# Performance work log

Measured on AMD Instinct MI355X. Metric: run time of the kernel, lower is better.

Reference implementation:

```python
import jax, jax.numpy as jnp
import numpy as np

N_NODES = 50000
N_EDGES = 800000
D_IN = 64
H1 = 64
H2 = 64
N_CLASSES = 10
N_GRAPHS = 500


def setup_inputs() -> dict:
    key = jax.random.key(0)
    ks = jax.random.split(key, 9)
    x = jax.random.normal(ks[0], (N_NODES, D_IN), dtype=jnp.float32)
    edge_index = jax.random.randint(ks[1], (2, N_EDGES), 0, N_NODES, dtype=jnp.int64)
    batch = jnp.sort(jax.random.randint(ks[2], (N_NODES,), 0, N_GRAPHS, dtype=jnp.int64))
    # Linear params (Kaiming-uniform-ish scale)
    def lin(k, fin, fout):
        kw, kb = jax.random.split(k)
        s = 1.0 / np.sqrt(fin)
        W = jax.random.uniform(kw, (fin, fout), minval=-s, maxval=s, dtype=jnp.float32)
        b = jax.random.uniform(kb, (fout,), minval=-s, maxval=s, dtype=jnp.float32)
        return W, b
    W1, b1 = lin(ks[3], D_IN, H1)
    W2, b2 = lin(ks[4], H1, H2)
    W3, b3 = lin(ks[5], H2, N_CLASSES)
    return {"x": x, "edge_index": edge_index, "batch": batch,
            "W1": W1, "b1": b1, "W2": W2, "b2": b2, "W3": W3, "b3": b3}


def _gin_conv(h, src, dst, W, b, eps=0.0):
    # sum aggregation of neighbor messages: msg[i] = sum_{(j->i)} h[j]
    agg = jax.ops.segment_sum(h[src], dst, num_segments=N_NODES)
    return ((1.0 + eps) * h + agg) @ W + b


def reference(x, edge_index, batch, W1, b1, W2, b2, W3, b3):
    src, dst = edge_index[0], edge_index[1]
    h = jax.nn.relu(_gin_conv(x, src, dst, W1, b1))
    h = jax.nn.relu(_gin_conv(h, src, dst, W2, b2))
    # global mean pool over graphs
    sums = jax.ops.segment_sum(h, batch, num_segments=N_GRAPHS)
    cnt = jax.ops.segment_sum(jnp.ones((N_NODES,), dtype=h.dtype), batch, num_segments=N_GRAPHS)
    pooled = sums / jnp.maximum(cnt, 1.0)[:, None]
    return pooled @ W3 + b3
```

## Files before the change

### kernel.cpp

```cpp
#include <hip/hip_runtime.h>
#include <hip/hip_bf16.h>
#include <hip/hip_fp16.h>


#define N_FEAT 64
#define CHUNK 4096
#define CAP 6144

typedef _Float16 f16;
typedef _Float16 half8 __attribute__((ext_vector_type(8)));
typedef float float4v __attribute__((ext_vector_type(4)));
typedef unsigned short u16;

__device__ inline f16 cvt_f16(float v) { return (f16)v; }
__device__ inline f16 cvt_f16(f16 v) { return v; }

template <typename TIN>
__device__ __forceinline__ void gemm_body(const TIN* __restrict__ X, const float* __restrict__ W,
                                          f16* __restrict__ Z, int nrows, int bidx, char* smemc) {
    f16 (*sX)[72] = (f16 (*)[72])smemc;
    f16 (*sWT)[72] = (f16 (*)[72])(smemc + 64 * 72 * sizeof(f16));
    int t = threadIdx.x;
    int base = bidx * 64;
    for (int idx = t; idx < 4096; idx += 256) {
        int k = idx >> 6, n = idx & 63;
        sWT[n][k] = (f16)W[idx];
    }
    for (int idx = t; idx < 4096; idx += 256) {
        int r = idx >> 6, c = idx & 63;
        int row = base + r;
        sX[r][c] = (row < nrows) ? cvt_f16(X[(size_t)row * 64 + c]) : (f16)0.f;
    }
    __syncthreads();
    int wave = t >> 6;
    int lane = t & 63;
    int quad = lane >> 4;
    int m16 = lane & 15;
    half8 a0 = *(const half8*)&sX[wave * 16 + m16][quad * 8];
    half8 a1 = *(const half8*)&sX[wave * 16 + m16][32 + quad * 8];
    float4v acc[4];
#pragma unroll
    for (int C = 0; C < 4; ++C) {
        half8 b0 = *(const half8*)&sWT[C * 16 + m16][quad * 8];
        half8 b1 = *(const half8*)&sWT[C * 16 + m16][32 + quad * 8];
        float4v d = {0.f, 0.f, 0.f, 0.f};
        d = __builtin_amdgcn_mfma_f32_16x16x32_f16(a0, b0, d, 0, 0, 0);
        d = __builtin_amdgcn_mfma_f32_16x16x32_f16(a1, b1, d, 0, 0, 0);
        acc[C] = d;
    }
#pragma unroll
    for (int reg = 0; reg < 4; ++reg) {
        int row = base + wave * 16 + quad * 4 + reg;
        if (row < nrows) {
#pragma unroll
            for (int C = 0; C < 4; ++C)
                Z[(size_t)row * 64 + C * 16 + m16] = (f16)acc[C][reg];
        }
    }
}

__global__ __launch_bounds__(256) void bucket_scatter(const int* __restrict__ src, const int* __restrict__ dst,
                               int* __restrict__ ccur, int* __restrict__ staging, int E) {
    __shared__ int epack[CHUNK];
    __shared__ int ebkt[CHUNK];
    __shared__ int hist[256];
    __shared__ int base[256];
    int t = threadIdx.x;
    int begin = blockIdx.x * CHUNK;
    int cnt = min(CHUNK, E - begin);
    hist[t] = 0;
    __syncthreads();
    for (int i = t; i < cnt; i += 256) {
        int d = dst[begin + i];
        int s = src[begin + i];
        epack[i] = (s & 0xFFFF) | ((d & 255) << 16);
        ebkt[i] = d >> 8;
        atomicAdd(&hist[d >> 8], 1);
    }
    __syncthreads();
    int h = hist[t];
    if (h > 0) base[t] = atomicAdd(&ccur[t], h);
    hist[t] = 0;
    __syncthreads();
    for (int i = t; i < cnt; i += 256) {
        int b = ebkt[i];
        int off = base[b] + atomicAdd(&hist[b], 1);
        if (off < CAP) staging[(size_t)b * CAP + off] = epack[i];
    }
}

__device__ __forceinline__ void finalize_body(const int* __restrict__ staging, const int* __restrict__ ccur,
                                              int2* __restrict__ rowse, u16* __restrict__ col, int N,
                                              int b, char* smemc) {
    int* edges = (int*)smemc;
    int* hist = edges + CAP;
    int* scan = hist + 256;
    int* cur = scan + 256;
    int t = threadIdx.x;
    int cnt = min(ccur[b], CAP);
    int sbase = b * CAP;
    hist[t] = 0;
    __syncthreads();
    for (int i = t; i < cnt; i += 256) {
        int e = staging[(size_t)sbase + i];
        edges[i] = e;
        atomicAdd(&hist[(e >> 16) & 255], 1);
    }
    __syncthreads();
    int v = hist[t];
    scan[t] = v;
    __syncthreads();
    for (int off = 1; off < 256; off <<= 1) {
        int u = (t >= off) ? scan[t - off] : 0;
        __syncthreads();
        scan[t] += u;
        __syncthreads();
    }
    int excl = scan[t] - v;
    cur[t] = excl;
    int node = b * 256 + t;
    if (node < N) rowse[node] = make_int2(sbase + excl, sbase + excl + v);
    __syncthreads();
    for (int i = t; i < cnt; i += 256) {
        int e = edges[i];
        int pos = sbase + atomicAdd(&cur[(e >> 16) & 255], 1);
        col[pos] = (u16)(e & 0xFFFF);
    }
}

__global__ __launch_bounds__(256) void fused_finalize_gemm(
        const int* __restrict__ staging, const int* __restrict__ ccur,
        int2* __restrict__ rowse, u16* __restrict__ col, int N,
        const float* __restrict__ X, const float* __restrict__ W,
        f16* __restrict__ Z, int nrows, int nbf) {
    __shared__ __align__(16) char smem[(CAP + 768) * 4];
    if ((int)blockIdx.x < nbf)
        finalize_body(staging, ccur, rowse, col, N, blockIdx.x, smem);
    else
        gemm_body<float>(X, W, Z, nrows, blockIdx.x - nbf, smem);
}

__global__ __launch_bounds__(512) void gather_gemm(
        const f16* __restrict__ Z, const int2* __restrict__ rowse,
        const u16* __restrict__ col, const float* __restrict__ bias,
        const float* __restrict__ W2, f16* __restrict__ Z2, int n) {
    __shared__ f16 sH[32][72];
    __shared__ f16 sWT[64][72];
    int t = threadIdx.x;
    for (int idx = t; idx < 4096; idx += 512) {
        int k = idx >> 6, nn = idx & 63;
        sWT[nn][k] = (f16)W2[idx];
    }
    int w = t >> 6;
    int lane = t & 63;
    int e = lane >> 3, c = lane & 7;
    int base = blockIdx.x * 32;
    const float4v* Z4 = reinterpret_cast<const float4v*>(Z);
    const float4* B4 = reinterpret_cast<const float4*>(bias);
#pragma unroll
    for (int q = 0; q < 4; ++q) {
        int node = base + w * 4 + q;
        bool valid = node < n;
        int lo = 0, hi = 0;
        if (valid) { int2 se = rowse[node]; lo = se.x; hi = se.y; }
        float acc[8] = {0.f, 0.f, 0.f, 0.f, 0.f, 0.f, 0.f, 0.f};
        int idx4[4];
#pragma unroll
        for (int i = 0; i < 4; ++i) {
            int j = lo + e + i * 8;
            idx4[i] = (j < hi) ? (int)col[j] : -1;
        }
#pragma unroll
        for (int i = 0; i < 4; ++i) {
            if (idx4[i] >= 0) {
                float4v r = Z4[(size_t)idx4[i] * 8 + c];
                half8 hv = *(half8*)&r;
#pragma unroll
                for (int k = 0; k < 8; ++k) acc[k] += (float)hv[k];
            }
        }
        for (int j = lo + 32 + e; j < hi; j += 8) {
            float4v r = Z4[(size_t)(int)col[j] * 8 + c];
            half8 hv = *(half8*)&r;
#pragma unroll
            for (int k = 0; k < 8; ++k) acc[k] += (float)hv[k];
        }
#pragma unroll
        for (int k = 0; k < 8; ++k) {
            acc[k] += __shfl_xor(acc[k], 8);
            acc[k] += __shfl_xor(acc[k], 16);
            acc[k] += __shfl_xor(acc[k], 32);
        }
        if (e == 0) {
            half8 o;
            if (valid) {
                float4v sr = Z4[(size_t)node * 8 + c];
                half8 sv = *(half8*)&sr;
                float4 b0 = B4[c * 2];
                float4 b1 = B4[c * 2 + 1];
                float bb[8] = {b0.x, b0.y, b0.z, b0.w, b1.x, b1.y, b1.z, b1.w};
#pragma unroll
                for (int k = 0; k < 8; ++k)
                    o[k] = (f16)fmaxf((float)sv[k] + acc[k] + bb[k], 0.f);
            } else {
#pragma unroll
                for (int k = 0; k < 8; ++k) o[k] = (f16)0.f;
            }
            *(half8*)&sH[w * 4 + q][c * 8] = o;
        }
    }
    __syncthreads();
    int quad = lane >> 4;
    int m16 = lane & 15;
    int mrow = (w >> 2) * 16;
    int ncol = (w & 3) * 16;
    half8 a0 = *(const half8*)&sH[mrow + m16][quad * 8];
    half8 a1 = *(const half8*)&sH[mrow + m16][32 + quad * 8];
    half8 b0 = *(const half8*)&sWT[ncol + m16][quad * 8];
    half8 b1 = *(const half8*)&sWT[ncol + m16][32 + quad * 8];
    float4v d = {0.f, 0.f, 0.f, 0.f};
    d = __builtin_amdgcn_mfma_f32_16x16x32_f16(a0, b0, d, 0, 0, 0);
    d = __builtin_amdgcn_mfma_f32_16x16x32_f16(a1, b1, d, 0, 0, 0);
#pragma unroll
    for (int reg = 0; reg < 4; ++reg) {
        int row = base + mrow + quad * 4 + reg;
        if (row < n)
            Z2[(size_t)row * 64 + ncol + m16] = (f16)d[reg];
    }
}

__global__ __launch_bounds__(256) void gather_pool(
        const f16* __restrict__ Z, const int2* __restrict__ rowse,
        const u16* __restrict__ col, const float* __restrict__ bias,
        float* __restrict__ sums, const int* __restrict__ batch, int n) {
    __shared__ float sh[4][64];
    __shared__ int gid[4];
    int w = threadIdx.x >> 6;
    int node = (int)(blockIdx.x * 4 + w);
    int lane = threadIdx.x & 63;
    int e = lane >> 3, c = lane & 7;
    bool valid = node < n;
    int lo = 0, hi = 0;
    if (valid) { int2 se = rowse[node]; lo = se.x; hi = se.y; }
    const float4v* Z4 = reinterpret_cast<const float4v*>(Z);
    float acc[8] = {0.f, 0.f, 0.f, 0.f, 0.f, 0.f, 0.f, 0.f};
    int idx[4];
#pragma unroll
    for (int i = 0; i < 4; ++i) {
        int j = lo + e + i * 8;
        idx[i] = (j < hi) ? (int)col[j] : -1;
    }
#pragma unroll
    for (int i = 0; i < 4; ++i) {
        if (idx[i] >= 0) {
            float4v r = Z4[(size_t)idx[i] * 8 + c];
            half8 hv = *(half8*)&r;
#pragma unroll
            for (int k = 0; k < 8; ++k) acc[k] += (float)hv[k];
        }
    }
    for (int j = lo + 32 + e; j < hi; j += 8) {
        float4v r = Z4[(size_t)(int)col[j] * 8 + c];
        half8 hv = *(half8*)&r;
#pragma unroll
        for (int k = 0; k < 8; ++k) acc[k] += (float)hv[k];
    }
#pragma unroll
    for (int k = 0; k < 8; ++k) {
        acc[k] += __shfl_xor(acc[k], 8);
        acc[k] += __shfl_xor(acc[k], 16);
        acc[k] += __shfl_xor(acc[k], 32);
    }
    if (lane == 0) gid[w] = valid ? batch[node] : -1;
    if (valid && e == 0) {
        float4v sr = Z4[(size_t)node * 8 + c];
        half8 sv = *(half8*)&sr;
        const float4* B4 = reinterpret_cast<const float4*>(bias);
        float4 b0 = B4[c * 2];
        float4 b1 = B4[c * 2 + 1];
        float bb[8] = {b0.x, b0.y, b0.z, b0.w, b1.x, b1.y, b1.z, b1.w};
#pragma unroll
        for (int k = 0; k < 8; ++k)
            sh[w][c * 8 + k] = fmaxf((float)sv[k] + acc[k] + bb[k], 0.f);
    }
    __syncthreads();
    if (w == 0) {
        int cg = gid[0];
        float run = 0.f;
#pragma unroll
        for (int q = 0; q < 4; ++q) {
            int g = gid[q];
            if (g < 0) break;
            if (g != cg) {
                atomicAdd(&sums[cg * 64 + lane], run);
                run = 0.f;
                cg = g;
            }
            run += sh[q][lane];
        }
        if (cg >= 0) atomicAdd(&sums[cg * 64 + lane], run);
    }
}

__global__ __launch_bounds__(64) void head_kernel(
        const float* __restrict__ sums, const int* __restrict__ batch,
        const float* __restrict__ W3, const float* __restrict__ b3,
        float* __restrict__ out, int n, int ncls) {
    int g = blockIdx.x;
    __shared__ float row[64];
    __shared__ int bnd[2];
    int t = threadIdx.x;
    if (t < 2) {
        int target = g + t;
        int lo = 0, hi = n;
        while (lo < hi) { int m = (lo + hi) >> 1; if (batch[m] < target) lo = m + 1; else hi = m; }
        bnd[t] = lo;
    }
    __syncthreads();
    float cnt = fmaxf((float)(bnd[1] - bnd[0]), 1.0f);
    row[t] = sums[g * 64 + t] / cnt;
    __syncthreads();
    if (t < ncls) {
        float o = b3[t];
#pragma unroll
        for (int k = 0; k < 64; ++k) o += row[k] * W3[k * ncls + t];
        out[g * ncls + t] = o;
    }
}

extern "C" void kernel_launch(void* const* d_in, const int* in_sizes, int n_in,
                              void* d_out, int out_size, void* d_ws, size_t ws_size,
                              hipStream_t stream) {
    const float* x     = (const float*)d_in[0];
    const int*   ei    = (const int*)d_in[1];
    const int*   batch = (const int*)d_in[2];
    const float* W1    = (const float*)d_in[3];
    const float* b1    = (const float*)d_in[4];
    const float* W2    = (const float*)d_in[5];
    const float* b2    = (const float*)d_in[6];
    const float* W3    = (const float*)d_in[7];
    const float* b3    = (const float*)d_in[8];
    float* out = (float*)d_out;

    const int N = in_sizes[0] / N_FEAT;
    const int E = in_sizes[1] / 2;
    const int NCLS = 10;
    const int G = out_size / NCLS;
    const int* src = ei;
    const int* dst = ei + E;
    const int nb = (N + 255) / 256;

    int*   staging = (int*)d_ws;
    int2*  rowse   = (int2*)(staging + (size_t)nb * CAP);
    u16*   col     = (u16*)(rowse + N);
    size_t colInts = ((size_t)nb * CAP * 2 + 15) / 16 * 4;
    int*   ccur    = (int*)(rowse + N) + colInts;
    float* sums    = (float*)(ccur + 256);
    f16*   zbuf    = (f16*)(sums + (size_t)G * 64);
    f16*   z2buf   = zbuf + (size_t)N * 64;

    const int gemmGrid = (N + 63) / 64;
    const int gg2Grid  = (N + 31) / 32;
    const int gatherGrid = (N + 3) / 4;
    const int scatGrid = (E + CHUNK - 1) / CHUNK;

    hipMemsetAsync(ccur, 0, (256 + (size_t)G * 64) * sizeof(int), stream);
    bucket_scatter<<<scatGrid, 256, 0, stream>>>(src, dst, ccur, staging, E);

    fused_finalize_gemm<<<nb + gemmGrid, 256, 0, stream>>>(
        staging, ccur, rowse, col, N, x, W1, zbuf, N, nb);

    gather_gemm<<<gg2Grid, 512, 0, stream>>>(zbuf, rowse, col, b1, W2, z2buf, N);

    gather_pool<<<gatherGrid, 256, 0, stream>>>(z2buf, rowse, col, b2, sums, batch, N);

    head_kernel<<<G, 64, 0, stream>>>(sums, batch, W3, b3, out, N, NCLS);
}
```

Before: 167.2 us.

## Fuse all GIN stages into one cooperative persistent kernel with grid syncs

Replaces the five separate launches (scatter, finalize+gemm, gather+gemm, gather+pool, head) with a single cooperative persistent kernel that loops over work units per stage and separates stages with grid.sync. The goal is to remove launch gaps and tail effects between the kernels. Layer-2 tiles shrink to 16 nodes per 256-thread block and scatter chunks to 2048 edges. In exchange, occupancy is capped by the mega kernel's large shared memory footprint, and each grid barrier has a cost. A fallback multi-kernel path is kept.

After: 514.2 us. +207.5%, slower.

```diff
diff --git a/kernel.cpp b/kernel.cpp
--- a/kernel.cpp
+++ b/kernel.cpp
@@ -1,10 +1,14 @@
 #include <hip/hip_runtime.h>
+#include <hip/hip_cooperative_groups.h>
 #include <hip/hip_bf16.h>
 #include <hip/hip_fp16.h>
 
+namespace cg = cooperative_groups;
+
 
 #define N_FEAT 64
 #define CHUNK 4096
+#define CHUNK_M 2048
 #define CAP 6144
 
 typedef _Float16 f16;
@@ -59,15 +63,17 @@
     }
 }
 
-__global__ __launch_bounds__(256) void bucket_scatter(const int* __restrict__ src, const int* __restrict__ dst,
-                               int* __restrict__ ccur, int* __restrict__ staging, int E) {
-    __shared__ int epack[CHUNK];
-    __shared__ int ebkt[CHUNK];
-    __shared__ int hist[256];
-    __shared__ int base[256];
-    int t = threadIdx.x;
-    int begin = blockIdx.x * CHUNK;
-    int cnt = min(CHUNK, E - begin);
+template <int CHSZ>
+__device__ __forceinline__ void scatter_body(const int* __restrict__ src, const int* __restrict__ dst,
+                                             int* __restrict__ ccur, int* __restrict__ staging,
+                                             int E, int bidx, char* smemc) {
+    int* epack = (int*)smemc;
+    int* ebkt  = epack + CHSZ;
+    int* hist  = ebkt + CHSZ;
+    int* base  = hist + 256;
+    int t = threadIdx.x;
+    int begin = bidx * CHSZ;
+    int cnt = min(CHSZ, E - begin);
     hist[t] = 0;
     __syncthreads();
     for (int i = t; i < cnt; i += 256) {
@@ -126,6 +132,227 @@
         int pos = sbase + atomicAdd(&cur[(e >> 16) & 255], 1);
         col[pos] = (u16)(e & 0xFFFF);
     }
+}
+
+__device__ __forceinline__ void gather_core(const float4v* __restrict__ Z4,
+                                            const u16* __restrict__ col,
+                                            int lo, int hi, int e, int c, float* acc) {
+    int idx4[4];
+#pragma unroll
+    for (int i = 0; i < 4; ++i) {
+        int j = lo + e + i * 8;
+        idx4[i] = (j < hi) ? (int)col[j] : -1;
+    }
+#pragma unroll
+    for (int i = 0; i < 4; ++i) {
+        if (idx4[i] >= 0) {
+            float4v r = Z4[(size_t)idx4[i] * 8 + c];
+            half8 hv = *(half8*)&r;
+#pragma unroll
+            for (int k = 0; k < 8; ++k) acc[k] += (float)hv[k];
+        }
+    }
+    for (int j = lo + 32 + e; j < hi; j += 8) {
+        float4v r = Z4[(size_t)(int)col[j] * 8 + c];
+        half8 hv = *(half8*)&r;
+#pragma unroll
+        for (int k = 0; k < 8; ++k) acc[k] += (float)hv[k];
+    }
+#pragma unroll
+    for (int k = 0; k < 8; ++k) {
+        acc[k] += __shfl_xor(acc[k], 8);
+        acc[k] += __shfl_xor(acc[k], 16);
+        acc[k] += __shfl_xor(acc[k], 32);
+    }
+}
+
+__device__ __forceinline__ void tile2_body(const f16* __restrict__ Z, const int2* __restrict__ rowse,
+                                           const u16* __restrict__ col, const float* __restrict__ bias,
+                                           f16* __restrict__ Z2, int n, int tile, char* smemc) {
+    f16 (*sH)[72] = (f16 (*)[72])smemc;
+    f16 (*sWT)[72] = (f16 (*)[72])(smemc + 16 * 72 * sizeof(f16));
+    int t = threadIdx.x;
+    int w = t >> 6, lane = t & 63, e = lane >> 3, c = lane & 7;
+    int base = tile * 16;
+    const float4v* Z4 = reinterpret_cast<const float4v*>(Z);
+    const float4* B4 = reinterpret_cast<const float4*>(bias);
+#pragma unroll
+    for (int q = 0; q < 4; ++q) {
+        int node = base + w * 4 + q;
+        bool valid = node < n;
+        int lo = 0, hi = 0;
+        if (valid) { int2 se = rowse[node]; lo = se.x; hi = se.y; }
+        float acc[8] = {0.f, 0.f, 0.f, 0.f, 0.f, 0.f, 0.f, 0.f};
+        gather_core(Z4, col, lo, hi, e, c, acc);
+        if (e == 0) {
+            half8 o;
+            if (valid) {
+                float4v sr = Z4[(size_t)node * 8 + c];
+                half8 sv = *(half8*)&sr;
+                float4 b0 = B4[c * 2];
+                float4 b1 = B4[c * 2 + 1];
+                float bb[8] = {b0.x, b0.y, b0.z, b0.w, b1.x, b1.y, b1.z, b1.w};
+#pragma unroll
+                for (int k = 0; k < 8; ++k)
+                    o[k] = (f16)fmaxf((float)sv[k] + acc[k] + bb[k], 0.f);
+            } else {
+#pragma unroll
+                for (int k = 0; k < 8; ++k) o[k] = (f16)0.f;
+            }
+            *(half8*)&sH[w * 4 + q][c * 8] = o;
+        }
+    }
+    __syncthreads();
+    int quad = lane >> 4;
+    int m16 = lane & 15;
+    half8 a0 = *(const half8*)&sH[m16][quad * 8];
+    half8 a1 = *(const half8*)&sH[m16][32 + quad * 8];
+    half8 b0 = *(const half8*)&sWT[w * 16 + m16][quad * 8];
+    half8 b1 = *(const half8*)&sWT[w * 16 + m16][32 + quad * 8];
+    float4v d = {0.f, 0.f, 0.f, 0.f};
+    d = __builtin_amdgcn_mfma_f32_16x16x32_f16(a0, b0, d, 0, 0, 0);
+    d = __builtin_amdgcn_mfma_f32_16x16x32_f16(a1, b1, d, 0, 0, 0);
+#pragma unroll
+    for (int reg = 0; reg < 4; ++reg) {
+        int row = base + quad * 4 + reg;
+        if (row < n)
+            Z2[(size_t)row * 64 + w * 16 + m16] = (f16)d[reg];
+    }
+}
+
+__device__ __forceinline__ void pool_unit_body(const f16* __restrict__ Z, const int2* __restrict__ rowse,
+                                               const u16* __restrict__ col, const float* __restrict__ bias,
+                                               float* __restrict__ sums, const int* __restrict__ batch,
+                                               int n, int u, char* smemc) {
+    float (*sh)[64] = (float (*)[64])smemc;
+    int* gid = (int*)(smemc + 4 * 64 * sizeof(float));
+    int w = threadIdx.x >> 6;
+    int node = u * 4 + w;
+    int lane = threadIdx.x & 63;
+    int e = lane >> 3, c = lane & 7;
+    bool valid = node < n;
+    int lo = 0, hi = 0;
+    if (valid) { int2 se = rowse[node]; lo = se.x; hi = se.y; }
+    const float4v* Z4 = reinterpret_cast<const float4v*>(Z);
+    float acc[8] = {0.f, 0.f, 0.f, 0.f, 0.f, 0.f, 0.f, 0.f};
+    gather_core(Z4, col, lo, hi, e, c, acc);
+    if (lane == 0) gid[w] = valid ? batch[node] : -1;
+    if (valid && e == 0) {
+        float4v sr = Z4[(size_t)node * 8 + c];
+        half8 sv = *(half8*)&sr;
+        const float4* B4 = reinterpret_cast<const float4*>(bias);
+        float4 b0 = B4[c * 2];
+        float4 b1 = B4[c * 2 + 1];
+        float bb[8] = {b0.x, b0.y, b0.z, b0.w, b1.x, b1.y, b1.z, b1.w};
+#pragma unroll
+        for (int k = 0; k < 8; ++k)
+            sh[w][c * 8 + k] = fmaxf((float)sv[k] + acc[k] + bb[k], 0.f);
+    }
+    __syncthreads();
+    if (w == 0) {
+        int cg = gid[0];
+        float run = 0.f;
+#pragma unroll
+        for (int q = 0; q < 4; ++q) {
+            int g = gid[q];
+            if (g < 0) break;
+            if (g != cg) {
+                atomicAdd(&sums[cg * 64 + lane], run);
+                run = 0.f;
+                cg = g;
+            }
+            run += sh[q][lane];
+        }
+        if (cg >= 0) atomicAdd(&sums[cg * 64 + lane], run);
+    }
+}
+
+__device__ __forceinline__ void head_body(const float* __restrict__ sums, const int* __restrict__ batch,
+                                          const float* __restrict__ W3, const float* __restrict__ b3,
+                                          float* __restrict__ out, int n, int ncls, int g, char* smemc) {
+    float* row = (float*)smemc;
+    int* bnd = (int*)(row + 64);
+    int t = threadIdx.x;
+    if (t < 2) {
+        int target = g + t;
+        int lo = 0, hi = n;
+        while (lo < hi) { int m = (lo + hi) >> 1; if (batch[m] < target) lo = m + 1; else hi = m; }
+        bnd[t] = lo;
+    }
+    __syncthreads();
+    if (t < 64) {
+        float cnt = fmaxf((float)(bnd[1] - bnd[0]), 1.0f);
+        row[t] = sums[g * 64 + t] / cnt;
+    }
+    __syncthreads();
+    if (t < ncls) {
+        float o = b3[t];
+#pragma unroll
+        for (int k = 0; k < 64; ++k) o += row[k] * W3[k * ncls + t];
+        out[g * ncls + t] = o;
+    }
+}
+
+struct MegaArgs {
+    const int* src; const int* dst; int* ccur; int* staging; int E;
+    const float* x; const float* W1; f16* zbuf;
+    int2* rowse; u16* col; int N;
+    const float* b1; const float* W2; f16* z2buf;
+    const float* b2; float* sums; const int* batch;
+    const float* W3; const float* b3; float* out; int G; int ncls;
+    int nscat; int nfin; int ngemm1; int ntile2; int nunit3;
+};
+
+__global__ __launch_bounds__(256) void gin_mega(MegaArgs a) {
+    __shared__ __align__(16) char smem[(CAP + 768) * 4];
+    cg::grid_group grid = cg::this_grid();
+    int nblk = gridDim.x, bid = blockIdx.x;
+
+    for (int ch = bid; ch < a.nscat; ch += nblk) {
+        scatter_body<CHUNK_M>(a.src, a.dst, a.ccur, a.staging, a.E, ch, smem);
+        __syncthreads();
+    }
+    grid.sync();
+
+    int nwork1 = a.nfin + a.ngemm1;
+    for (int u = bid; u < nwork1; u += nblk) {
+        if (u < a.nfin) finalize_body(a.staging, a.ccur, a.rowse, a.col, a.N, u, smem);
+        else            gemm_body<float>(a.x, a.W1, a.zbuf, a.N, u - a.nfin, smem);
+        __syncthreads();
+    }
+    grid.sync();
+
+    {
+        f16 (*sWT)[72] = (f16 (*)[72])(smem + 16 * 72 * sizeof(f16));
+        int t = threadIdx.x;
+        for (int idx = t; idx < 4096; idx += 256) {
+            int k = idx >> 6, nn = idx & 63;
+            sWT[nn][k] = (f16)a.W2[idx];
+        }
+        __syncthreads();
+        for (int tile = bid; tile < a.ntile2; tile += nblk) {
+            tile2_body(a.zbuf, a.rowse, a.col, a.b1, a.z2buf, a.N, tile, smem);
+            __syncthreads();
+        }
+    }
+    grid.sync();
+
+    for (int u = bid; u < a.nunit3; u += nblk) {
+        pool_unit_body(a.z2buf, a.rowse, a.col, a.b2, a.sums, a.batch, a.N, u, smem);
+        __syncthreads();
+    }
+    grid.sync();
+
+    for (int g = bid; g < a.G; g += nblk) {
+        head_body(a.sums, a.batch, a.W3, a.b3, a.out, a.N, a.ncls, g, smem);
+        __syncthreads();
+    }
+}
+
+__global__ __launch_bounds__(256) void bucket_scatter(const int* __restrict__ src, const int* __restrict__ dst,
+                               int* __restrict__ ccur, int* __restrict__ staging, int E) {
+    __shared__ __align__(16) char smem[(CHUNK * 2 + 512) * 4];
+    scatter_body<CHUNK>(src, dst, ccur, staging, E, blockIdx.x, smem);
 }
 
 __global__ __launch_bounds__(256) void fused_finalize_gemm(
@@ -140,192 +367,35 @@
         gemm_body<float>(X, W, Z, nrows, blockIdx.x - nbf, smem);
 }
 
-__global__ __launch_bounds__(512) void gather_gemm(
+__global__ __launch_bounds__(256) void gather_gemm16(
         const f16* __restrict__ Z, const int2* __restrict__ rowse,
         const u16* __restrict__ col, const float* __restrict__ bias,
         const float* __restrict__ W2, f16* __restrict__ Z2, int n) {
-    __shared__ f16 sH[32][72];
-    __shared__ f16 sWT[64][72];
-    int t = threadIdx.x;
-    for (int idx = t; idx < 4096; idx += 512) {
+    __shared__ __align__(16) char smem[16 * 72 * 2 + 64 * 72 * 2];
+    f16 (*sWT)[72] = (f16 (*)[72])(smem + 16 * 72 * sizeof(f16));
+    int t = threadIdx.x;
+    for (int idx = t; idx < 4096; idx += 256) {
         int k = idx >> 6, nn = idx & 63;
         sWT[nn][k] = (f16)W2[idx];
     }
-    int w = t >> 6;
-    int lane = t & 63;
-    int e = lane >> 3, c = lane & 7;
-    int base = blockIdx.x * 32;
-    const float4v* Z4 = reinterpret_cast<const float4v*>(Z);
-    const float4* B4 = reinterpret_cast<const float4*>(bias);
-#pragma unroll
-    for (int q = 0; q < 4; ++q) {
-        int node = base + w * 4 + q;
-        bool valid = node < n;
-        int lo = 0, hi = 0;
-        if (valid) { int2 se = rowse[node]; lo = se.x; hi = se.y; }
-        float acc[8] = {0.f, 0.f, 0.f, 0.f, 0.f, 0.f, 0.f, 0.f};
-        int idx4[4];
-#pragma unroll
-        for (int i = 0; i < 4; ++i) {
-            int j = lo + e + i * 8;
-            idx4[i] = (j < hi) ? (int)col[j] : -1;
-        }
-#pragma unroll
-        for (int i = 0; i < 4; ++i) {
-            if (idx4[i] >= 0) {
-                float4v r = Z4[(size_t)idx4[i] * 8 + c];
-                half8 hv = *(half8*)&r;
-#pragma unroll
-                for (int k = 0; k < 8; ++k) acc[k] += (float)hv[k];
-            }
-        }
-        for (int j = lo + 32 + e; j < hi; j += 8) {
-            float4v r = Z4[(size_t)(int)col[j] * 8 + c];
-            half8 hv = *(half8*)&r;
-#pragma unroll
-            for (int k = 0; k < 8; ++k) acc[k] += (float)hv[k];
-        }
-#pragma unroll
-        for (int k = 0; k < 8; ++k) {
-            acc[k] += __shfl_xor(acc[k], 8);
-            acc[k] += __shfl_xor(acc[k], 16);
-            acc[k] += __shfl_xor(acc[k], 32);
-        }
-        if (e == 0) {
-            half8 o;
-            if (valid) {
-                float4v sr = Z4[(size_t)node * 8 + c];
-                half8 sv = *(half8*)&sr;
-                float4 b0 = B4[c * 2];
-                float4 b1 = B4[c * 2 + 1];
-                float bb[8] = {b0.x, b0.y, b0.z, b0.w, b1.x, b1.y, b1.z, b1.w};
-#pragma unroll
-                for (int k = 0; k < 8; ++k)
-                    o[k] = (f16)fmaxf((float)sv[k] + acc[k] + bb[k], 0.f);
-            } else {
-#pragma unroll
-                for (int k = 0; k < 8; ++k) o[k] = (f16)0.f;
-            }
-            *(half8*)&sH[w * 4 + q][c * 8] = o;
-        }
-    }
-    __syncthreads();
-    int quad = lane >> 4;
-    int m16 = lane & 15;
-    int mrow = (w >> 2) * 16;
-    int ncol = (w & 3) * 16;
-    half8 a0 = *(const half8*)&sH[mrow + m16][quad * 8];
-    half8 a1 = *(const half8*)&sH[mrow + m16][32 + quad * 8];
-    half8 b0 = *(const half8*)&sWT[ncol + m16][quad * 8];
-    half8 b1 = *(const half8*)&sWT[ncol + m16][32 + quad * 8];
-    float4v d = {0.f, 0.f, 0.f, 0.f};
-    d = __builtin_amdgcn_mfma_f32_16x16x32_f16(a0, b0, d, 0, 0, 0);
-    d = __builtin_amdgcn_mfma_f32_16x16x32_f16(a1, b1, d, 0, 0, 0);
-#pragma unroll
-    for (int reg = 0; reg < 4; ++reg) {
-        int row = base + mrow + quad * 4 + reg;
-        if (row < n)
-            Z2[(size_t)row * 64 + ncol + m16] = (f16)d[reg];
-    }
+    __syncthreads();
+    tile2_body(Z, rowse, col, bias, Z2, n, blockIdx.x, smem);
 }
 
 __global__ __launch_bounds__(256) void gather_pool(
         const f16* __restrict__ Z, const int2* __restrict__ rowse,
         const u16* __restrict__ col, const float* __restrict__ bias,
         float* __restrict__ sums, const int* __restrict__ batch, int n) {
-    __shared__ float sh[4][64];
-    __shared__ int gid[4];
-    int w = threadIdx.x >> 6;
-    int node = (int)(blockIdx.x * 4 + w);
-    int lane = threadIdx.x & 63;
-    int e = lane >> 3, c = lane & 7;
-    bool valid = node < n;
-    int lo = 0, hi = 0;
-    if (valid) { int2 se = rowse[node]; lo = se.x; hi = se.y; }
-    const float4v* Z4 = reinterpret_cast<const float4v*>(Z);
-    float acc[8] = {0.f, 0.f, 0.f, 0.f, 0.f, 0.f, 0.f, 0.f};
-    int idx[4];
-#pragma unroll
-    for (int i = 0; i < 4; ++i) {
-        int j = lo + e + i * 8;
-        idx[i] = (j < hi) ? (int)col[j] : -1;
-    }
-#pragma unroll
-    for (int i = 0; i < 4; ++i) {
-        if (idx[i] >= 0) {
-            float4v r = Z4[(size_t)idx[i] * 8 + c];
-            half8 hv = *(half8*)&r;
-#pragma unroll
-            for (int k = 0; k < 8; ++k) acc[k] += (float)hv[k];
-        }
-    }
-    for (int j = lo + 32 + e; j < hi; j += 8) {
-        float4v r = Z4[(size_t)(int)col[j] * 8 + c];
-        half8 hv = *(half8*)&r;
-#pragma unroll
-        for (int k = 0; k < 8; ++k) acc[k] += (float)hv[k];
-    }
-#pragma unroll
-    for (int k = 0; k < 8; ++k) {
-        acc[k] += __shfl_xor(acc[k], 8);
-        acc[k] += __shfl_xor(acc[k], 16);
-        acc[k] += __shfl_xor(acc[k], 32);
-    }
-    if (lane == 0) gid[w] = valid ? batch[node] : -1;
-    if (valid && e == 0) {
-        float4v sr = Z4[(size_t)node * 8 + c];
-        half8 sv = *(half8*)&sr;
-        const float4* B4 = reinterpret_cast<const float4*>(bias);
-        float4 b0 = B4[c * 2];
-        float4 b1 = B4[c * 2 + 1];
-        float bb[8] = {b0.x, b0.y, b0.z, b0.w, b1.x, b1.y, b1.z, b1.w};
-#pragma unroll
-        for (int k = 0; k < 8; ++k)
-            sh[w][c * 8 + k] = fmaxf((float)sv[k] + acc[k] + bb[k], 0.f);
-    }
-    __syncthreads();
-    if (w == 0) {
-        int cg = gid[0];
-        float run = 0.f;
-#pragma unroll
-        for (int q = 0; q < 4; ++q) {
-            int g = gid[q];
-            if (g < 0) break;
-            if (g != cg) {
-                atomicAdd(&sums[cg * 64 + lane], run);
-                run = 0.f;
-                cg = g;
-            }
-            run += sh[q][lane];
-        }
-        if (cg >= 0) atomicAdd(&sums[cg * 64 + lane], run);
-    }
-}
-
-__global__ __launch_bounds__(64) void head_kernel(
+    __shared__ __align__(16) char smem[4 * 64 * 4 + 16];
+    pool_unit_body(Z, rowse, col, bias, sums, batch, n, blockIdx.x, smem);
+}
+
+__global__ __launch_bounds__(256) void head_kernel(
         const float* __restrict__ sums, const int* __restrict__ batch,
         const float* __restrict__ W3, const float* __restrict__ b3,
         float* __restrict__ out, int n, int ncls) {
-    int g = blockIdx.x;
-    __shared__ float row[64];
-    __shared__ int bnd[2];
-    int t = threadIdx.x;
-    if (t < 2) {
-        int target = g + t;
-        int lo = 0, hi = n;
-        while (lo < hi) { int m = (lo + hi) >> 1; if (batch[m] < target) lo = m + 1; else hi = m; }
-        bnd[t] = lo;
-    }
-    __syncthreads();
-    float cnt = fmaxf((float)(bnd[1] - bnd[0]), 1.0f);
-    row[t] = sums[g * 64 + t] / cnt;
-    __syncthreads();
-    if (t < ncls) {
-        float o = b3[t];
-#pragma unroll
-        for (int k = 0; k < 64; ++k) o += row[k] * W3[k * ncls + t];
-        out[g * ncls + t] = o;
-    }
+    __shared__ __align__(16) char smem[64 * 4 + 16];
+    head_body(sums, batch, W3, b3, out, n, ncls, blockIdx.x, smem);
 }
 
 extern "C" void kernel_launch(void* const* d_in, const int* in_sizes, int n_in,
@@ -360,19 +430,56 @@
     f16*   z2buf   = zbuf + (size_t)N * 64;
 
     const int gemmGrid = (N + 63) / 64;
-    const int gg2Grid  = (N + 31) / 32;
+    const int tile2Grid = (N + 15) / 16;
     const int gatherGrid = (N + 3) / 4;
     const int scatGrid = (E + CHUNK - 1) / CHUNK;
+    const int nscatM = (E + CHUNK_M - 1) / CHUNK_M;
+
+    static int coopGrid = -2;
+    if (coopGrid == -2) {
+        int dev = 0; hipGetDevice(&dev);
+        int can = 0;
+        hipDeviceGetAttribute(&can, hipDeviceAttributeCooperativeLaunch, dev);
+        if (can) {
+            int mb = 0;
+            hipError_t oe = hipOccupancyMaxActiveBlocksPerMultiprocessor(
+                &mb, reinterpret_cast<const void*>(gin_mega), 256, 0);
+            int cus = 0;
+            hipDeviceGetAttribute(&cus, hipDeviceAttributeMultiprocessorCount, dev);
+            if (oe == hipSuccess && mb > 0 && cus > 0) {
+                coopGrid = mb * cus;
+                if (coopGrid > 2048) coopGrid = 2048;
+            } else coopGrid = -1;
+        } else coopGrid = -1;
+    }
 
     hipMemsetAsync(ccur, 0, (256 + (size_t)G * 64) * sizeof(int), stream);
-    bucket_scatter<<<scatGrid, 256, 0, stream>>>(src, dst, ccur, staging, E);
-
-    fused_finalize_gemm<<<nb + gemmGrid, 256, 0, stream>>>(
-        staging, ccur, rowse, col, N, x, W1, zbuf, N, nb);
-
-    gather_gemm<<<gg2Grid, 512, 0, stream>>>(zbuf, rowse, col, b1, W2, z2buf, N);
-
-    gather_pool<<<gatherGrid, 256, 0, stream>>>(z2buf, rowse, col, b2, sums, batch, N);
-
-    head_kernel<<<G, 64, 0, stream>>>(sums, batch, W3, b3, out, N, NCLS);
-}
+
+    bool done = false;
+    if (coopGrid > 0) {
+        MegaArgs a;
+        a.src = src; a.dst = dst; a.ccur = ccur; a.staging = staging; a.E = E;
+        a.x = x; a.W1 = W1; a.zbuf = zbuf;
+        a.rowse = rowse; a.col = col; a.N = N;
+        a.b1 = b1; a.W2 = W2; a.z2buf = z2buf;
+        a.b2 = b2; a.sums = sums; a.batch = batch;
+        a.W3 = W3; a.b3 = b3; a.out = out; a.G = G; a.ncls = NCLS;
+        a.nscat = nscatM; a.nfin = nb; a.ngemm1 = gemmGrid;
+        a.ntile2 = tile2Grid; a.nunit3 = gatherGrid;
+        void* kargs[] = { &a };
+        hipError_t e = hipLaunchCooperativeKernel(
+            reinterpret_cast<const void*>(gin_mega),
+            dim3(coopGrid), dim3(256), kargs, 0u, stream);
+        if (e == hipSuccess) done = true;
+        else coopGrid = -1;
+    }
+
+    if (!done) {
+        bucket_scatter<<<scatGrid, 256, 0, stream>>>(src, dst, ccur, staging, E);
+        fused_finalize_gemm<<<nb + gemmGrid, 256, 0, stream>>>(
+            staging, ccur, rowse, col, N, x, W1, zbuf, N, nb);
+        gather_gemm16<<<tile2Grid, 256, 0, stream>>>(zbuf, rowse, col, b1, W2, z2buf, N);
+        gather_pool<<<gatherGrid, 256, 0, stream>>>(z2buf, rowse, col, b2, sums, batch, N);
+        head_kernel<<<G, 256, 0, stream>>>(sums, batch, W3, b3, out, N, NCLS);
+    }
+}
```

## Split first-layer GEMM across scatter and finalize kernels, fold sums zeroing in

Applied to the files above, without the earlier changes.

The bucket-scatter kernel becomes a fused kernel whose extra blocks compute the first 304 row-tiles of the layer-1 GEMM, and the finalize kernel computes the remaining tiles. This spreads the GEMM work so it overlaps both graph-preprocessing phases and fills idle CUs during the scatter. Zeroing of the pooled sums buffer moves from the memset into extra blocks of the finalize kernel, shrinking the memset to the bucket counters. The split point is a hard-coded constant tuned to this problem size and CU count, and the scatter kernel now carries a shared-memory footprint sized for both bodies.

Result: no change. 167.4 us (+0.1%).

```diff
diff --git a/kernel.cpp b/kernel.cpp
--- a/kernel.cpp
+++ b/kernel.cpp
@@ -59,14 +59,15 @@
     }
 }
 
-__global__ __launch_bounds__(256) void bucket_scatter(const int* __restrict__ src, const int* __restrict__ dst,
-                               int* __restrict__ ccur, int* __restrict__ staging, int E) {
-    __shared__ int epack[CHUNK];
-    __shared__ int ebkt[CHUNK];
-    __shared__ int hist[256];
-    __shared__ int base[256];
+__device__ __forceinline__ void scatter_body(const int* __restrict__ src, const int* __restrict__ dst,
+                                             int* __restrict__ ccur, int* __restrict__ staging,
+                                             int E, int bidx, char* smemc) {
+    int* epack = (int*)smemc;
+    int* ebkt  = epack + CHUNK;
+    int* hist  = ebkt + CHUNK;
+    int* base  = hist + 256;
     int t = threadIdx.x;
-    int begin = blockIdx.x * CHUNK;
+    int begin = bidx * CHUNK;
     int cnt = min(CHUNK, E - begin);
     hist[t] = 0;
     __syncthreads();
@@ -128,16 +129,37 @@
     }
 }
 
+__global__ __launch_bounds__(256) void fused_scatter_gemm(
+        const int* __restrict__ src, const int* __restrict__ dst,
+        int* __restrict__ ccur, int* __restrict__ staging, int E,
+        const float* __restrict__ X, const float* __restrict__ W,
+        f16* __restrict__ Z, int nrows, int nsb) {
+    __shared__ __align__(16) char smem[(CHUNK * 2 + 512) * 4];
+    if ((int)blockIdx.x < nsb)
+        scatter_body(src, dst, ccur, staging, E, blockIdx.x, smem);
+    else
+        gemm_body<float>(X, W, Z, nrows, blockIdx.x - nsb, smem);
+}
+
 __global__ __launch_bounds__(256) void fused_finalize_gemm(
         const int* __restrict__ staging, const int* __restrict__ ccur,
         int2* __restrict__ rowse, u16* __restrict__ col, int N,
         const float* __restrict__ X, const float* __restrict__ W,
-        f16* __restrict__ Z, int nrows, int nbf) {
+        f16* __restrict__ Z, int nrows, int nbf, int g1a, int ng1b,
+        float* __restrict__ sums, int sumsN) {
     __shared__ __align__(16) char smem[(CAP + 768) * 4];
-    if ((int)blockIdx.x < nbf)
-        finalize_body(staging, ccur, rowse, col, N, blockIdx.x, smem);
-    else
-        gemm_body<float>(X, W, Z, nrows, blockIdx.x - nbf, smem);
+    int b = blockIdx.x;
+    if (b < nbf) {
+        finalize_body(staging, ccur, rowse, col, N, b, smem);
+    } else if (b < nbf + ng1b) {
+        gemm_body<float>(X, W, Z, nrows, (b - nbf) + g1a, smem);
+    } else {
+        int zb = b - nbf - ng1b;
+        float4* s4 = (float4*)sums;
+        int n4 = sumsN >> 2;
+        for (int i = zb * 256 + threadIdx.x; i < n4; i += 8 * 256)
+            s4[i] = make_float4(0.f, 0.f, 0.f, 0.f);
+    }
 }
 
 __global__ __launch_bounds__(512) void gather_gemm(
@@ -363,12 +385,18 @@
     const int gg2Grid  = (N + 31) / 32;
     const int gatherGrid = (N + 3) / 4;
     const int scatGrid = (E + CHUNK - 1) / CHUNK;
-
-    hipMemsetAsync(ccur, 0, (256 + (size_t)G * 64) * sizeof(int), stream);
-    bucket_scatter<<<scatGrid, 256, 0, stream>>>(src, dst, ccur, staging, E);
-
-    fused_finalize_gemm<<<nb + gemmGrid, 256, 0, stream>>>(
-        staging, ccur, rowse, col, N, x, W1, zbuf, N, nb);
+    const int g1a = 304;
+    const int g1b = gemmGrid - g1a;
+    const int zblk = 8;
+
+    hipMemsetAsync(ccur, 0, 256 * sizeof(int), stream);
+
+    fused_scatter_gemm<<<scatGrid + g1a, 256, 0, stream>>>(
+        src, dst, ccur, staging, E, x, W1, zbuf, N, scatGrid);
+
+    fused_finalize_gemm<<<nb + g1b + zblk, 256, 0, stream>>>(
+        staging, ccur, rowse, col, N, x, W1, zbuf, N, nb, g1a, g1b,
+        sums, G * 64);
 
     gather_gemm<<<gg2Grid, 512, 0, stream>>>(zbuf, rowse, col, b1, W2, z2buf, N);
 
```
